# Kernel optimization log

Measured on AMD Instinct MI355X. Metric: run time of the kernel, lower is better.

## Reference

```python
import jax, jax.numpy as jnp
import numpy as np

DIM, DH, H_HEADS, F, HH, WW = 512, 64, 8, 16, 32, 32
FF_IN = int(DIM * 4 * 2 / 3)  # 1365


def _ln(x, w, b):
    m = x.mean(-1, keepdims=True)
    v = ((x - m) ** 2).mean(-1, keepdims=True)
    return (x - m) * jax.lax.rsqrt(v + 1e-5) * w + b


def _attn(x, ln_w, ln_b, wq, wkv, nkv, nbias, wout, oln_w, oln_b, rel_bias):
    # x: (B, N, D); K/V are single-head (shared across heads) per the source to_kv
    B, N, D = x.shape
    H = nbias.shape[0]
    dh = nkv.shape[-1]
    xn = _ln(x, ln_w, ln_b)
    q = (xn @ wq).reshape(B, N, H, dh).transpose(0, 2, 1, 3) * (dh ** -0.5)
    k, v = jnp.split(xn @ wkv, 2, axis=-1)  # (B, N, dh) each
    nk = jnp.broadcast_to(nkv[0], (B, 1, dh))
    nv = jnp.broadcast_to(nkv[1], (B, 1, dh))
    k = jnp.concatenate([nk, k], axis=1)  # (B, N+1, dh)
    v = jnp.concatenate([nv, v], axis=1)
    sim = jnp.einsum('bhid,bjd->bhij', q, k)  # (B, H, N, N+1)
    bias = jnp.concatenate([jnp.broadcast_to(nbias[:, None, None], (H, N, 1)), rel_bias], axis=-1)
    attn = jax.nn.softmax(sim + bias[None], axis=-1)
    out = jnp.einsum('bhij,bjd->bhid', attn, v)
    out = out.transpose(0, 2, 1, 3).reshape(B, N, H * dh)
    return _ln(out @ wout, oln_w, oln_b)


def _cpb_mlp(coords, w0, b0, w1, b1, w2, b2):
    t = jax.nn.silu(coords @ w0 + b0)
    t = jax.nn.silu(t @ w1 + b1)
    return t @ w2 + b2  # (R, heads)


def _spatial_bias(h, w, w0, b0, w1, b1, w2, b2):
    rh = jnp.arange(-h + 1, h)
    rw = jnp.arange(-w + 1, w)
    gh, gw = jnp.meshgrid(rh, rw, indexing='ij')
    coords = jnp.stack([gh, gw], axis=-1).reshape(-1, 2).astype(jnp.float32)
    table = _cpb_mlp(coords, w0, b0, w1, b1, w2, b2)  # ((2h-1)(2w-1), H)
    ph, pw = jnp.meshgrid(jnp.arange(h), jnp.arange(w), indexing='ij')
    p = jnp.stack([ph, pw], axis=-1).reshape(-1, 2)  # (hw, 2)
    rel = p[:, None] - p[None]  # (hw, hw, 2)
    idx = (rel[..., 0] + h - 1) * (2 * w - 1) + (rel[..., 1] + w - 1)
    return table[idx].transpose(2, 0, 1)  # (H, hw, hw)


def _temporal_bias(f, w0, b0, w1, b1, w2, b2):
    coords = jnp.arange(-f + 1, f, dtype=jnp.float32)[:, None]
    table = _cpb_mlp(coords, w0, b0, w1, b1, w2, b2)  # (2f-1, H)
    idx = jnp.arange(f)[:, None] - jnp.arange(f)[None] + f - 1
    return table[idx].transpose(2, 0, 1)  # (H, f, f)


def _ff(x, win, g, wout):
    # 1x1x1 conv == channel matmul; GEGLU; shift_token; ChanLayerNorm; conv out
    y = jnp.einsum('bcfhw,cd->bdfhw', x, win)
    a, gate = jnp.split(y, 2, axis=1)
    y = a * jax.nn.gelu(gate, approximate=False)
    c = y.shape[1]
    c1 = (c + 1) // 2  # torch.chunk: first chunk gets ceil
    y1, y2 = y[:, :c1], y[:, c1:]
    y2 = jnp.pad(y2, ((0, 0), (0, 0), (1, 0), (0, 0), (0, 0)))[:, :, :-1]
    y = jnp.concatenate([y1, y2], axis=1)
    m = y.mean(1, keepdims=True)
    v = ((y - m) ** 2).mean(1, keepdims=True)
    y = (y - m) * jax.lax.rsqrt(jnp.maximum(v, 1e-5)) * g.reshape(1, -1, 1, 1, 1)
    return jnp.einsum('bcfhw,cd->bdfhw', y, wout)


def setup_inputs() -> dict:
    key = jax.random.key(0)
    ks = jax.random.split(key, 32)
    d2 = DIM // 2
    inner = DH * H_HEADS

    def nrm(k, shape, s=0.02):
        return jax.random.normal(k, shape, jnp.float32) * s

    inp = {'x': jax.random.normal(ks[0], (1, DIM, F, HH, WW), jnp.float32)}
    for pre, i in (('sa', 1), ('ta', 11)):
        inp[pre + '_ln_w'] = jnp.ones(DIM, jnp.float32)
        inp[pre + '_ln_b'] = jnp.zeros(DIM, jnp.float32)
        inp[pre + '_wq'] = nrm(ks[i], (DIM, inner))
        inp[pre + '_wkv'] = nrm(ks[i + 1], (DIM, 2 * DH))
        inp[pre + '_null_kv'] = nrm(ks[i + 2], (2, DH), 1.0)
        inp[pre + '_null_bias'] = nrm(ks[i + 3], (H_HEADS,), 1.0)
        inp[pre + '_wout'] = nrm(ks[i + 4], (inner, DIM))
        inp[pre + '_oln_w'] = jnp.ones(DIM, jnp.float32)
        inp[pre + '_oln_b'] = jnp.zeros(DIM, jnp.float32)
    inp['sp_w0'] = nrm(ks[20], (2, d2), 0.1); inp['sp_b0'] = jnp.zeros(d2, jnp.float32)
    inp['sp_w1'] = nrm(ks[21], (d2, d2), 0.05); inp['sp_b1'] = jnp.zeros(d2, jnp.float32)
    inp['sp_w2'] = nrm(ks[22], (d2, H_HEADS), 0.05); inp['sp_b2'] = jnp.zeros(H_HEADS, jnp.float32)
    inp['tp_w0'] = nrm(ks[23], (1, d2), 0.1); inp['tp_b0'] = jnp.zeros(d2, jnp.float32)
    inp['tp_w1'] = nrm(ks[24], (d2, d2), 0.05); inp['tp_b1'] = jnp.zeros(d2, jnp.float32)
    inp['tp_w2'] = nrm(ks[25], (d2, H_HEADS), 0.05); inp['tp_b2'] = jnp.zeros(H_HEADS, jnp.float32)
    inp['ff_win'] = nrm(ks[26], (DIM, 2 * FF_IN))
    inp['ff_g'] = jnp.ones(FF_IN, jnp.float32)
    inp['ff_wout'] = nrm(ks[27], (FF_IN, DIM))
    return inp


def _forward(x, sa_ln_w, sa_ln_b, sa_wq, sa_wkv, sa_null_kv, sa_null_bias, sa_wout, sa_oln_w, sa_oln_b,
             ta_ln_w, ta_ln_b, ta_wq, ta_wkv, ta_null_kv, ta_null_bias, ta_wout, ta_oln_w, ta_oln_b,
             sp_w0, sp_b0, sp_w1, sp_b1, sp_w2, sp_b2,
             tp_w0, tp_b0, tp_w1, tp_b1, tp_w2, tp_b2,
             ff_win, ff_g, ff_wout):
    b, c, f, h, w = x.shape
    # spatial attention over (h*w) tokens, batched over (b*f)
    xs = x.transpose(0, 2, 3, 4, 1).reshape(b * f, h * w, c)
    sb = _spatial_bias(h, w, sp_w0, sp_b0, sp_w1, sp_b1, sp_w2, sp_b2)
    xs = _attn(xs, sa_ln_w, sa_ln_b, sa_wq, sa_wkv, sa_null_kv, sa_null_bias, sa_wout, sa_oln_w, sa_oln_b, sb) + xs
    xv = xs.reshape(b, f, h, w, c).transpose(0, 4, 1, 2, 3)
    # temporal attention over f tokens, batched over (b*h*w)
    xt = xv.transpose(0, 3, 4, 2, 1).reshape(b * h * w, f, c)
    tb = _temporal_bias(f, tp_w0, tp_b0, tp_w1, tp_b1, tp_w2, tp_b2)
    xt = _attn(xt, ta_ln_w, ta_ln_b, ta_wq, ta_wkv, ta_null_kv, ta_null_bias, ta_wout, ta_oln_w, ta_oln_b, tb) + xt
    xv = xt.reshape(b, h, w, f, c).transpose(0, 4, 3, 1, 2)
    # feed-forward with token shift
    return _ff(xv, ff_win, ff_g, ff_wout) + xv


def reference(x, sa_ln_w, sa_ln_b, sa_wq, sa_wkv, sa_null_kv, sa_null_bias, sa_wout, sa_oln_w, sa_oln_b,
              ta_ln_w, ta_ln_b, ta_wq, ta_wkv, ta_null_kv, ta_null_bias, ta_wout, ta_oln_w, ta_oln_b,
              sp_w0, sp_b0, sp_w1, sp_b1, sp_w2, sp_b2,
              tp_w0, tp_b0, tp_w1, tp_b1, tp_w2, tp_b2,
              ff_win, ff_g, ff_wout):
    return _forward(x, sa_ln_w, sa_ln_b, sa_wq, sa_wkv, sa_null_kv, sa_null_bias, sa_wout, sa_oln_w, sa_oln_b,
                    ta_ln_w, ta_ln_b, ta_wq, ta_wkv, ta_null_kv, ta_null_bias, ta_wout, ta_oln_w, ta_oln_b,
                    sp_w0, sp_b0, sp_w1, sp_b1, sp_w2, sp_b2,
                    tp_w0, tp_b0, tp_w1, tp_b1, tp_w2, tp_b2,
                    ff_win, ff_g, ff_wout)
```

## Files before the change

kernel.cpp:

```cpp
#include <hip/hip_runtime.h>
#include <math.h>

#define TOK 16384
#define DIMC 512
#define FFI 1365
#define CH1 683
#define YSLD 1376
#define KVPAD 1056
#define BSTRIDE 1152
#define MASKB (-30000.f)
#define LOG2E 1.4426950408889634f

typedef unsigned int u32;
typedef unsigned short ushort_t;
typedef __attribute__((ext_vector_type(8))) short bf16x8;
typedef __attribute__((ext_vector_type(4))) float f32x4;

__device__ inline ushort_t f2b(float x) {
    u32 u = __float_as_uint(x);
    u32 r = (u + 0x7fffu + ((u >> 16) & 1u)) >> 16;
    return (ushort_t)r;
}
__device__ inline float b2f(ushort_t u) { return __uint_as_float(((u32)u) << 16); }

__device__ inline float exp2_fast(float x) {
    float r;
    asm("v_exp_f32 %0, %1" : "=v"(r) : "v"(x));
    return r;
}

__device__ inline u32 cvt_pk_bf16(float lo, float hi) {
    u32 r;
    asm("v_cvt_pk_bf16_f32 %0, %1, %2" : "=v"(r) : "v"(lo), "v"(hi));
    return r;
}

__device__ inline void gload_lds16(const void* g, void* l) {
    __builtin_amdgcn_global_load_lds(
        (const __attribute__((address_space(1))) u32*)g,
        (__attribute__((address_space(3))) u32*)l, 16, 0, 0);
}

__device__ inline float gelu_exact(float x) {
    return 0.5f * x * (1.f + erff(x * 0.70710678118654752f));
}

__device__ inline void waitcnt_vm4() {
    asm volatile("s_waitcnt vmcnt(4)" ::: "memory");
    __builtin_amdgcn_sched_barrier(0);
}
__device__ inline void waitcnt_vm0() {
    asm volatile("s_waitcnt vmcnt(0)" ::: "memory");
    __builtin_amdgcn_sched_barrier(0);
}

__global__ __launch_bounds__(256) void cpb_kernel(
    const float* __restrict__ w0, const float* __restrict__ b0,
    const float* __restrict__ w1, const float* __restrict__ b1,
    const float* __restrict__ w2, const float* __restrict__ b2,
    float* __restrict__ table, int mode, int nrows)
{
    __shared__ float t0[16][256];
    __shared__ float t1[16][256];
    int r0 = blockIdx.x * 16;
    int t = threadIdx.x;
    float w0t = w0[t], b0t = b0[t];
    float w0t2 = (mode == 0) ? w0[256 + t] : 0.f;
    #pragma unroll
    for (int rr = 0; rr < 16; ++rr) {
        int r = r0 + rr; if (r >= nrows) r = nrows - 1;
        float c0, c1;
        if (mode == 0) { c0 = (float)(r / 63 - 31); c1 = (float)(r % 63 - 31); }
        else           { c0 = (float)(r - 15);      c1 = 0.f; }
        float a = c0 * w0t + b0t;
        if (mode == 0) a += c1 * w0t2;
        t0[rr][t] = a / (1.f + __expf(-a));
    }
    __syncthreads();
    float b1t = b1[t];
    float acc[16];
    #pragma unroll
    for (int rr = 0; rr < 16; ++rr) acc[rr] = b1t;
    for (int k = 0; k < 256; ++k) {
        float w = w1[k * 256 + t];
        #pragma unroll
        for (int rr = 0; rr < 16; ++rr) acc[rr] += t0[rr][k] * w;
    }
    #pragma unroll
    for (int rr = 0; rr < 16; ++rr) {
        float s = acc[rr];
        t1[rr][t] = s / (1.f + __expf(-s));
    }
    __syncthreads();
    if (t < 128) {
        int rr = t >> 3, oo = t & 7;
        int r = r0 + rr;
        if (r < nrows) {
            float o = b2[oo];
            for (int k = 0; k < 256; ++k) o += t1[rr][k] * w2[k * 8 + oo];
            table[r * 8 + oo] = o;
        }
    }
}

__global__ __launch_bounds__(256) void bias_sp_kernel(
    const float* __restrict__ tab, const float* __restrict__ nullbias,
    ushort_t* __restrict__ out)
{
    int pi = blockIdx.x, h = blockIdx.y;
    int phi = pi >> 5, pwi = pi & 31;
    ushort_t* row = out + ((size_t)h * 1024 + pi) * BSTRIDE;
    for (int c = threadIdx.x; c < BSTRIDE; c += 256) {
        float v;
        if (c == 0) v = nullbias[h];
        else if (c <= 1024) {
            int pj = c - 1;
            int phj = pj >> 5, pwj = pj & 31;
            int idx = (phi - phj + 31) * 63 + (pwi - pwj + 31);
            v = tab[idx * 8 + h];
        } else v = MASKB;
        row[c] = f2b(v * LOG2E);
    }
}

__global__ __launch_bounds__(256) void kvinit_kernel(
    const float* __restrict__ nullkv, ushort_t* __restrict__ KP, ushort_t* __restrict__ VT)
{
    int f = blockIdx.x, t = threadIdx.x;
    for (int e = t; e < 32 * 64; e += 256) {
        int rr = e >> 6, d = e & 63;
        int row = (rr == 0) ? 0 : (1024 + rr);
        KP[((size_t)f * KVPAD + row) * 64 + d] = (rr == 0) ? f2b(nullkv[d]) : (ushort_t)0;
    }
    for (int e = t; e < 64 * 32; e += 256) {
        int d = e >> 5, cc = e & 31;
        int col = (cc == 0) ? 0 : (1024 + cc);
        VT[((size_t)f * 64 + d) * KVPAD + col] = (cc == 0) ? f2b(nullkv[64 + d]) : (ushort_t)0;
    }
}

__global__ __launch_bounds__(256) void wcvt_kernel(
    const float* __restrict__ W, int ldw, int c0,
    ushort_t* __restrict__ Bt, int Kp, int K, int Ncols,
    const float* __restrict__ gv, int Nwrite)
{
    __shared__ float tile[32][33];
    int nb = blockIdx.x * 32, kb = blockIdx.y * 32;
    int tx = threadIdx.x & 31, ty = threadIdx.x >> 5;
    #pragma unroll
    for (int it = 0; it < 4; ++it) {
        int k = kb + ty + it * 8, n = nb + tx;
        float v = (k < K && n < Ncols) ? W[(size_t)k * ldw + c0 + n] : 0.f;
        if (gv && k < K) v *= gv[k];
        tile[ty + it * 8][tx] = v;
    }
    __syncthreads();
    #pragma unroll
    for (int it = 0; it < 4; ++it) {
        int n = nb + ty + it * 8, k = kb + tx;
        if (n < Nwrite && k < Kp) Bt[(size_t)n * Kp + k] = f2b(tile[tx][ty + it * 8]);
    }
}

__global__ __launch_bounds__(256) void transpose_in_kernel(
    const float* __restrict__ x, float* __restrict__ dst)
{
    __shared__ float tile[32][33];
    int t0b = blockIdx.x * 32, c0b = blockIdx.y * 32;
    int tx = threadIdx.x & 31, ty = threadIdx.x >> 5;
    #pragma unroll
    for (int it = 0; it < 4; ++it) {
        int c = ty + it * 8;
        tile[c][tx] = x[(size_t)(c0b + c) * TOK + t0b + tx];
    }
    __syncthreads();
    #pragma unroll
    for (int it = 0; it < 4; ++it) {
        int tr = ty + it * 8;
        dst[(size_t)(t0b + tr) * DIMC + c0b + tx] = tile[tx][tr];
    }
}

__global__ __launch_bounds__(256) void ln_bf16_kernel(
    const float* __restrict__ in, ushort_t* __restrict__ out,
    const float* __restrict__ w, const float* __restrict__ b)
{
    __shared__ float r1[4], r2[4];
    size_t base = (size_t)blockIdx.x * DIMC;
    int t = threadIdx.x;
    float x0 = in[base + t], x1 = in[base + 256 + t];
    float s = x0 + x1, s2 = x0 * x0 + x1 * x1;
    #pragma unroll
    for (int o = 32; o > 0; o >>= 1) { s += __shfl_down(s, o, 64); s2 += __shfl_down(s2, o, 64); }
    if ((t & 63) == 0) { r1[t >> 6] = s; r2[t >> 6] = s2; }
    __syncthreads();
    float mean = (r1[0] + r1[1] + r1[2] + r1[3]) * (1.f / 512.f);
    float ex2  = (r2[0] + r2[1] + r2[2] + r2[3]) * (1.f / 512.f);
    float rstd = rsqrtf(ex2 - mean * mean + 1e-5f);
    out[base + t]       = f2b((x0 - mean) * rstd * w[t] + b[t]);
    out[base + 256 + t] = f2b((x1 - mean) * rstd * w[256 + t] + b[256 + t]);
}

__global__ __launch_bounds__(256) void ln_add_sp_kernel(
    const float* __restrict__ proj, const float* __restrict__ resid,
    float* __restrict__ dstT, ushort_t* __restrict__ dstB,
    const float* __restrict__ w, const float* __restrict__ b,
    const float* __restrict__ lnw, const float* __restrict__ lnb)
{
    __shared__ float r1[4], r2[4];
    int s = blockIdx.x;
    size_t base = (size_t)s * DIMC;
    int t = threadIdx.x;
    float x0 = proj[base + t], x1 = proj[base + 256 + t];
    float sa = x0 + x1, s2 = x0 * x0 + x1 * x1;
    #pragma unroll
    for (int o = 32; o > 0; o >>= 1) { sa += __shfl_down(sa, o, 64); s2 += __shfl_down(s2, o, 64); }
    if ((t & 63) == 0) { r1[t >> 6] = sa; r2[t >> 6] = s2; }
    __syncthreads();
    float mean = (r1[0] + r1[1] + r1[2] + r1[3]) * (1.f / 512.f);
    float ex2  = (r2[0] + r2[1] + r2[2] + r2[3]) * (1.f / 512.f);
    float rstd = rsqrtf(ex2 - mean * mean + 1e-5f);
    int rd = (s & 1023) * 16 + (s >> 10);
    size_t ob = (size_t)rd * DIMC;
    float v0 = resid[base + t]       + (x0 - mean) * rstd * w[t] + b[t];
    float v1 = resid[base + 256 + t] + (x1 - mean) * rstd * w[256 + t] + b[256 + t];
    dstT[ob + t]       = v0;
    dstT[ob + 256 + t] = v1;
    __syncthreads();
    float sb = v0 + v1, sb2 = v0 * v0 + v1 * v1;
    #pragma unroll
    for (int o = 32; o > 0; o >>= 1) { sb += __shfl_down(sb, o, 64); sb2 += __shfl_down(sb2, o, 64); }
    if ((t & 63) == 0) { r1[t >> 6] = sb; r2[t >> 6] = sb2; }
    __syncthreads();
    float mean2 = (r1[0] + r1[1] + r1[2] + r1[3]) * (1.f / 512.f);
    float ex22  = (r2[0] + r2[1] + r2[2] + r2[3]) * (1.f / 512.f);
    float rstd2 = rsqrtf(ex22 - mean2 * mean2 + 1e-5f);
    dstB[ob + t]       = f2b((v0 - mean2) * rstd2 * lnw[t] + lnb[t]);
    dstB[ob + 256 + t] = f2b((v1 - mean2) * rstd2 * lnw[256 + t] + lnb[256 + t]);
}

__global__ __launch_bounds__(256) void ln_add_tp_kernel(
    const float* __restrict__ proj, const float* __restrict__ resid,
    float* __restrict__ dstF, ushort_t* __restrict__ dstB,
    const float* __restrict__ w, const float* __restrict__ b)
{
    __shared__ float r1[4], r2[4];
    int tt = blockIdx.x;
    size_t base = (size_t)tt * DIMC;
    int t = threadIdx.x;
    float x0 = proj[base + t], x1 = proj[base + 256 + t];
    float sa = x0 + x1, s2 = x0 * x0 + x1 * x1;
    #pragma unroll
    for (int o = 32; o > 0; o >>= 1) { sa += __shfl_down(sa, o, 64); s2 += __shfl_down(s2, o, 64); }
    if ((t & 63) == 0) { r1[t >> 6] = sa; r2[t >> 6] = s2; }
    __syncthreads();
    float mean = (r1[0] + r1[1] + r1[2] + r1[3]) * (1.f / 512.f);
    float ex2  = (r2[0] + r2[1] + r2[2] + r2[3]) * (1.f / 512.f);
    float rstd = rsqrtf(ex2 - mean * mean + 1e-5f);
    float v0 = resid[base + t]       + (x0 - mean) * rstd * w[t] + b[t];
    float v1 = resid[base + 256 + t] + (x1 - mean) * rstd * w[256 + t] + b[256 + t];
    int sd = (tt & 15) * 1024 + (tt >> 4);
    size_t ob = (size_t)sd * DIMC;
    dstF[ob + t]       = v0;
    dstF[ob + 256 + t] = v1;
    dstB[ob + t]       = f2b(v0);
    dstB[ob + 256 + t] = f2b(v1);
}

template<int EPI>
__global__ __launch_bounds__(256) void gemm_mfma(
    const ushort_t* __restrict__ A, int lda,
    const ushort_t* __restrict__ Bt, int Kp,
    float* __restrict__ C, ushort_t* __restrict__ Cb, int ldc,
    int M, int N, int K, float scale, int nx,
    const float* __restrict__ stats, const float* __restrict__ g,
    const float* __restrict__ resid, float* __restrict__ outT,
    ushort_t* __restrict__ KPo, ushort_t* __restrict__ VTo)
{
    __shared__ __align__(16) ushort_t As[2][4 * 128 * 8];
    __shared__ __align__(16) ushort_t Bs[2][4 * 128 * 8];
    int lin = blockIdx.x;
    int xcd = lin & 7, idx = lin >> 3;
    int m0 = (xcd * 16 + (idx & 15)) * 128;
    int n0 = (idx >> 4) * 128;
    int tid = threadIdx.x, lane = tid & 63, wid = tid >> 6;
    int wy = wid >> 1, wx = wid & 1, quad = lane >> 4, l16 = lane & 15;
    bool bfull = (n0 + 128 <= N);
    f32x4 acc[4][4];
    #pragma unroll
    for (int i = 0; i < 4; ++i)
        #pragma unroll
        for (int j = 0; j < 4; ++j) { acc[i][j][0]=0.f; acc[i][j][1]=0.f; acc[i][j][2]=0.f; acc[i][j][3]=0.f; }

    if (bfull) {
        int NT = K >> 5;
        int c0 = wid * 128 + lane, c1 = wid * 128 + 64 + lane;
        const ushort_t* gA0 = A + (size_t)(m0 + (c0 & 127)) * lda + (c0 >> 7) * 8;
        const ushort_t* gA1 = A + (size_t)(m0 + (c1 & 127)) * lda + (c1 >> 7) * 8;
        const ushort_t* gB0 = Bt + (size_t)(n0 + (c0 & 127)) * Kp + (c0 >> 7) * 8;
        const ushort_t* gB1 = Bt + (size_t)(n0 + (c1 & 127)) * Kp + (c1 >> 7) * 8;
        const int lo0 = (wid * 128) * 8, lo1 = (wid * 128 + 64) * 8;
        auto stage = [&](int buf) {
            gload_lds16(gA0, &As[buf][lo0]);
            gload_lds16(gA1, &As[buf][lo1]);
            gload_lds16(gB0, &Bs[buf][lo0]);
            gload_lds16(gB1, &Bs[buf][lo1]);
            gA0 += 32; gA1 += 32; gB0 += 32; gB1 += 32;
        };
        stage(0);
        if (NT > 1) stage(1);
        for (int t = 0; t < NT; ++t) {
            if (t + 1 < NT) waitcnt_vm4(); else waitcnt_vm0();
            __builtin_amdgcn_s_barrier();
            int cur = t & 1;
            bf16x8 af[4], bfr[4];
            #pragma unroll
            for (int i = 0; i < 4; ++i) af[i] = *(bf16x8*)&As[cur][(quad * 128 + wy * 64 + i * 16 + l16) * 8];
            #pragma unroll
            for (int j = 0; j < 4; ++j) bfr[j] = *(bf16x8*)&Bs[cur][(quad * 128 + wx * 64 + j * 16 + l16) * 8];
            #pragma unroll
            for (int i = 0; i < 4; ++i)
                #pragma unroll
                for (int j = 0; j < 4; ++j)
                    acc[i][j] = __builtin_amdgcn_mfma_f32_16x16x32_bf16(af[i], bfr[j], acc[i][j], 0, 0, 0);
            if (t + 2 < NT) {
                __builtin_amdgcn_s_barrier();
                stage(cur);
            }
        }
    } else {
        for (int k0 = 0; k0 < K; k0 += 32) {
            if (k0) __syncthreads();
            #pragma unroll
            for (int r = 0; r < 2; ++r) {
                int c = wid * 128 + r * 64 + lane;
                const ushort_t* src = A + (size_t)(m0 + (c & 127)) * lda + k0 + (c >> 7) * 8;
                gload_lds16(src, &As[0][(wid * 128 + r * 64) * 8]);
            }
            #pragma unroll
            for (int r = 0; r < 2; ++r) {
                int c = tid + r * 256;
                int kg = c >> 7, nloc = c & 127;
                bf16x8 v;
                if (n0 + nloc < N) v = *(const bf16x8*)(Bt + (size_t)(n0 + nloc) * Kp + k0 + kg * 8);
                else { for (int e = 0; e < 8; ++e) v[e] = 0; }
                *(bf16x8*)&Bs[0][c * 8] = v;
            }
            __syncthreads();
            bf16x8 af[4], bfr[4];
            #pragma unroll
            for (int i = 0; i < 4; ++i) af[i] = *(bf16x8*)&As[0][(quad * 128 + wy * 64 + i * 16 + l16) * 8];
            #pragma unroll
            for (int j = 0; j < 4; ++j) bfr[j] = *(bf16x8*)&Bs[0][(quad * 128 + wx * 64 + j * 16 + l16) * 8];
            #pragma unroll
            for (int i = 0; i < 4; ++i)
                #pragma unroll
                for (int j = 0; j < 4; ++j)
                    acc[i][j] = __builtin_amdgcn_mfma_f32_16x16x32_bf16(af[i], bfr[j], acc[i][j], 0, 0, 0);
        }
    }
    #pragma unroll
    for (int i = 0; i < 4; ++i) {
        #pragma unroll
        for (int j = 0; j < 4; ++j) {
            #pragma unroll
            for (int r = 0; r < 4; ++r) {
                int m = m0 + wy * 64 + i * 16 + quad * 4 + r;
                int n = n0 + wx * 64 + j * 16 + l16;
                if (n >= N) continue;
                float raw = acc[i][j][r];
                float v = raw * scale;
                if (EPI == 0) {
                    C[(size_t)m * ldc + n] = v;
                } else if (EPI == 3) {
                    Cb[(size_t)m * ldc + n] = f2b(v);
                } else if (EPI == 5) {
                    float s0 = stats[2 * m], s1 = stats[2 * m + 1];
                    outT[(size_t)n * TOK + m] = v * s1 - s0 * g[n] + resid[(size_t)m * DIMC + n];
                } else if (EPI == 6) {
                    if (n < 512) {
                        Cb[(size_t)m * 512 + n] = f2b(v);
                    } else {
                        int frame = m >> 10, tt = m & 1023;
                        int d = n - 512;
                        if (d < 64) KPo[((size_t)frame * KVPAD + 1 + tt) * 64 + d] = f2b(raw);
                        else        VTo[((size_t)frame * 64 + (d - 64)) * KVPAD + 1 + tt] = f2b(raw);
                    }
                } else if (EPI == 7) {
                    if (n < 512) Cb[(size_t)m * 512 + n] = f2b(v);
                    else         KPo[(size_t)m * 128 + (n - 512)] = f2b(raw);
                }
            }
        }
    }
}

__global__ __launch_bounds__(256) void ff_gemm_fused(
    const ushort_t* __restrict__ A,
    const ushort_t* __restrict__ BI,
    ushort_t* __restrict__ YS)
{
    __shared__ __align__(16) ushort_t As[2][4 * 128 * 8];
    __shared__ __align__(16) ushort_t Bs[2][4 * 2 * 64 * 8];
    int lin = blockIdx.x;
    int xcd = lin & 7, idx = lin >> 3;
    int m0 = (xcd * 16 + (idx & 15)) * 128;
    int n0 = (idx >> 4) * 64;
    int tid = threadIdx.x, lane = tid & 63, wid = tid >> 6;
    int wy = wid >> 1, wx = wid & 1, quad = lane >> 4, l16 = lane & 15;
    f32x4 aA[4][2], aG[4][2];
    #pragma unroll
    for (int i = 0; i < 4; ++i)
        #pragma unroll
        for (int j = 0; j < 2; ++j) {
            aA[i][j][0]=0.f; aA[i][j][1]=0.f; aA[i][j][2]=0.f; aA[i][j][3]=0.f;
            aG[i][j][0]=0.f; aG[i][j][1]=0.f; aG[i][j][2]=0.f; aG[i][j][3]=0.f;
        }

    int c0 = wid * 128 + lane, c1 = wid * 128 + 64 + lane;
    const ushort_t* gA0 = A + (size_t)(m0 + (c0 & 127)) * 512 + (c0 >> 7) * 8;
    const ushort_t* gA1 = A + (size_t)(m0 + (c1 & 127)) * 512 + (c1 >> 7) * 8;
    const ushort_t* gB0 = BI + (size_t)((n0 + lane) * 2 + 0) * 512 + wid * 8;
    const ushort_t* gB1 = BI + (size_t)((n0 + lane) * 2 + 1) * 512 + wid * 8;
    const int lo0 = (wid * 128) * 8, lo1 = (wid * 128 + 64) * 8;
    auto stage = [&](int buf) {
        gload_lds16(gA0, &As[buf][lo0]);
        gload_lds16(gA1, &As[buf][lo1]);
        gload_lds16(gB0, &Bs[buf][lo0]);
        gload_lds16(gB1, &Bs[buf][lo1]);
        gA0 += 32; gA1 += 32; gB0 += 32; gB1 += 32;
    };

    stage(0); stage(1);
    for (int t = 0; t < 16; ++t) {
        if (t + 1 < 16) waitcnt_vm4(); else waitcnt_vm0();
        __builtin_amdgcn_s_barrier();
        int cur = t & 1;
        bf16x8 af[4], ba[2], bg[2];
        #pragma unroll
        for (int i = 0; i < 4; ++i) af[i] = *(bf16x8*)&As[cur][(quad * 128 + wy * 64 + i * 16 + l16) * 8];
        #pragma unroll
        for (int j = 0; j < 2; ++j) {
            int nn = wx * 32 + j * 16 + l16;
            ba[j] = *(bf16x8*)&Bs[cur][(quad * 128 + nn) * 8];
            bg[j] = *(bf16x8*)&Bs[cur][(quad * 128 + 64 + nn) * 8];
        }
        #pragma unroll
        for (int i = 0; i < 4; ++i)
            #pragma unroll
            for (int j = 0; j < 2; ++j) {
                aA[i][j] = __builtin_amdgcn_mfma_f32_16x16x32_bf16(af[i], ba[j], aA[i][j], 0, 0, 0);
                aG[i][j] = __builtin_amdgcn_mfma_f32_16x16x32_bf16(af[i], bg[j], aG[i][j], 0, 0, 0);
            }
        if (t + 2 < 16) {
            __builtin_amdgcn_s_barrier();
            stage(cur);
        }
    }
    #pragma unroll
    for (int i = 0; i < 4; ++i) {
        #pragma unroll
        for (int j = 0; j < 2; ++j) {
            #pragma unroll
            for (int r = 0; r < 4; ++r) {
                int m = m0 + wy * 64 + i * 16 + quad * 4 + r;
                int n = n0 + wx * 32 + j * 16 + l16;
                if (n >= FFI) {
                    if (n < YSLD) YS[(size_t)m * YSLD + n] = 0;
                    continue;
                }
                float v = aA[i][j][r] * gelu_exact(aG[i][j][r]);
                int dr = (n < CH1) ? m : m + 1024;
                if (dr < TOK) YS[(size_t)dr * YSLD + n] = f2b(v);
                if (n >= CH1 && m < 1024) YS[(size_t)m * YSLD + n] = 0;
            }
        }
    }
}

__global__ __launch_bounds__(256) void attn_sp_mfma(
    const ushort_t* __restrict__ Q,
    const ushort_t* __restrict__ KP,
    const ushort_t* __restrict__ VT,
    const ushort_t* __restrict__ BIASX,
    ushort_t* __restrict__ O)
{
    __shared__ __align__(16) ushort_t Ks[128 * 64];
    __shared__ __align__(16) ushort_t Vs[64 * 128];
    int lin = blockIdx.x;
    int xcd = lin & 7, idx = lin >> 3;
    int qt = xcd * 8 + (idx & 7);
    int frame = idx >> 3;
    int q0 = qt * 16;
    int tid = threadIdx.x, lane = tid & 63, wid = tid >> 6;
    int quad = lane >> 4, l16 = lane & 15;

    bf16x8 aQ[2][2];
    const ushort_t* brow[2];
    #pragma unroll
    for (int i = 0; i < 2; ++i) {
        int h = wid * 2 + i;
        const ushort_t* qp = Q + (size_t)(frame * 1024 + q0 + l16) * 512 + h * 64 + quad * 8;
        aQ[i][0] = *(const bf16x8*)qp;
        aQ[i][1] = *(const bf16x8*)(qp + 32);
        brow[i] = BIASX + ((size_t)h * 1024 + q0 + l16) * BSTRIDE;
    }
    f32x4 Oc[2][4];
    f32x4 Oc4[2];
    #pragma unroll
    for (int i = 0; i < 2; ++i) {
        #pragma unroll
        for (int nt = 0; nt < 4; ++nt) { Oc[i][nt][0]=0.f; Oc[i][nt][1]=0.f; Oc[i][nt][2]=0.f; Oc[i][nt][3]=0.f; }
        Oc4[i][0]=0.f; Oc4[i][1]=0.f; Oc4[i][2]=0.f; Oc4[i][3]=0.f;
    }
    bf16x8 vones;
    #pragma unroll
    for (int e = 0; e < 8; ++e) vones[e] = (short)0x3F80;

    int idxA = (((quad & 1) * 32) + l16) * 4;
    int idxB = idxA + 64;
    bool hiq = (quad >= 2);

    for (int jt = 0; jt < 9; ++jt) {
        __syncthreads();
        #pragma unroll
        for (int r = 0; r < 4; ++r) {
            int L = wid * 256 + r * 64 + lane;
            int c = L >> 3, gp = L & 7, gg = gp ^ (c & 7);
            int jj = jt * 128 + c; if (jj > KVPAD - 1) jj = KVPAD - 1;
            gload_lds16(KP + ((size_t)frame * KVPAD + jj) * 64 + gg * 8, &Ks[(wid * 256 + r * 64) * 8]);
        }
        #pragma unroll
        for (int r = 0; r < 4; ++r) {
            int L = wid * 256 + r * 64 + lane;
            int d = L >> 4, cgp = L & 15;
            int cg = (cgp & 8) | ((cgp & 7) ^ (d & 7));
            int col = jt * 128 + cg * 8; if (col > KVPAD - 8) col = KVPAD - 8;
            gload_lds16(VT + ((size_t)frame * 64 + d) * KVPAD + col, &Vs[(wid * 256 + r * 64) * 8]);
        }
        __syncthreads();

        #pragma unroll
        for (int i = 0; i < 2; ++i) {
            f32x4 S[8];
            #pragma unroll
            for (int j = 0; j < 8; ++j) { S[j][0]=0.f; S[j][1]=0.f; S[j][2]=0.f; S[j][3]=0.f; }
            __builtin_amdgcn_s_setprio(1);
            #pragma unroll
            for (int j = 0; j < 8; ++j) {
                int c = j * 16 + l16;
                #pragma unroll
                for (int ks = 0; ks < 2; ++ks) {
                    bf16x8 kb = *(bf16x8*)&Ks[(c * 8 + ((ks * 4 + quad) ^ (c & 7))) * 8];
                    S[j] = __builtin_amdgcn_mfma_f32_16x16x32_bf16(kb, aQ[i][ks], S[j], 0, 0, 0);
                }
            }
            __builtin_amdgcn_s_setprio(0);
            #pragma unroll
            for (int j = 0; j < 8; ++j) {
                int kbase = jt * 128 + j * 16 + quad * 4;
                uint2 bv = *(const uint2*)(brow[i] + kbase);
                S[j][0] = exp2_fast(S[j][0] + __uint_as_float(bv.x << 16));
                S[j][1] = exp2_fast(S[j][1] + __uint_as_float(bv.x & 0xffff0000u));
                S[j][2] = exp2_fast(S[j][2] + __uint_as_float(bv.y << 16));
                S[j][3] = exp2_fast(S[j][3] + __uint_as_float(bv.y & 0xffff0000u));
            }
            __builtin_amdgcn_s_setprio(1);
            #pragma unroll
            for (int ks = 0; ks < 4; ++ks) {
                int jl = 2 * ks, jh = 2 * ks + 1;
                u32 pxl = cvt_pk_bf16(S[jl][0], S[jl][1]);
                u32 pyl = cvt_pk_bf16(S[jl][2], S[jl][3]);
                u32 pxh = cvt_pk_bf16(S[jh][0], S[jh][1]);
                u32 pyh = cvt_pk_bf16(S[jh][2], S[jh][3]);
                u32 a0 = (u32)__builtin_amdgcn_ds_bpermute(idxA, (int)pxl);
                u32 a1 = (u32)__builtin_amdgcn_ds_bpermute(idxA, (int)pxh);
                u32 b0 = (u32)__builtin_amdgcn_ds_bpermute(idxA, (int)pyl);
                u32 b1 = (u32)__builtin_amdgcn_ds_bpermute(idxA, (int)pyh);
                u32 c0 = (u32)__builtin_amdgcn_ds_bpermute(idxB, (int)pxl);
                u32 c1 = (u32)__builtin_amdgcn_ds_bpermute(idxB, (int)pxh);
                u32 d0 = (u32)__builtin_amdgcn_ds_bpermute(idxB, (int)pyl);
                u32 d1 = (u32)__builtin_amdgcn_ds_bpermute(idxB, (int)pyh);
                union { u32 w[4]; bf16x8 v; } pa;
                pa.w[0] = hiq ? a1 : a0;
                pa.w[1] = hiq ? b1 : b0;
                pa.w[2] = hiq ? c1 : c0;
                pa.w[3] = hiq ? d1 : d0;
                #pragma unroll
                for (int nt = 0; nt < 4; ++nt) {
                    int d = nt * 16 + l16;
                    int cg = ks * 4 + quad;
                    int phys = (cg & 8) | ((cg & 7) ^ (d & 7));
                    bf16x8 vb = *(bf16x8*)&Vs[(d * 16 + phys) * 8];
                    Oc[i][nt] = __builtin_amdgcn_mfma_f32_16x16x32_bf16(pa.v, vb, Oc[i][nt], 0, 0, 0);
                }
                Oc4[i] = __builtin_amdgcn_mfma_f32_16x16x32_bf16(pa.v, vones, Oc4[i], 0, 0, 0);
            }
            __builtin_amdgcn_s_setprio(0);
        }
    }
    #pragma unroll
    for (int i = 0; i < 2; ++i) {
        int h = wid * 2 + i;
        #pragma unroll
        for (int r = 0; r < 4; ++r) {
            float linv = 1.f / Oc4[i][r];
            int ql = quad * 4 + r;
            #pragma unroll
            for (int nt = 0; nt < 4; ++nt) {
                int d = nt * 16 + l16;
                O[(size_t)(frame * 1024 + q0 + ql) * 512 + h * 64 + d] = f2b(Oc[i][nt][r] * linv);
            }
        }
    }
}

__global__ __launch_bounds__(256) void attn_tp_kernel(
    const ushort_t* __restrict__ q, const ushort_t* __restrict__ kv,
    const float* __restrict__ nullkv, const float* __restrict__ nullbias,
    const float* __restrict__ table, ushort_t* __restrict__ out)
{
    __shared__ float qs[16][516];
    __shared__ float ks[17][68];
    __shared__ float vs[17][68];
    __shared__ float sc[8][16][17];
    int b = blockIdx.x;
    int t = threadIdx.x;
    for (int e = t; e < 16 * 64; e += 256) {
        int f = e >> 6, c8 = e & 63;
        uint4 v = *(const uint4*)(q + (size_t)(b * 16 + f) * 512 + c8 * 8);
        float* dst = &qs[f][c8 * 8];
        dst[0] = b2f((ushort_t)(v.x & 0xffffu)); dst[1] = b2f((ushort_t)(v.x >> 16));
        dst[2] = b2f((ushort_t)(v.y & 0xffffu)); dst[3] = b2f((ushort_t)(v.y >> 16));
        dst[4] = b2f((ushort_t)(v.z & 0xffffu)); dst[5] = b2f((ushort_t)(v.z >> 16));
        dst[6] = b2f((ushort_t)(v.w & 0xffffu)); dst[7] = b2f((ushort_t)(v.w >> 16));
    }
    for (int e = t; e < 17 * 64; e += 256) {
        int j = e >> 6, d = e & 63;
        ks[j][d] = (j == 0) ? nullkv[d]      : b2f(kv[(size_t)(b * 16 + j - 1) * 128 + d]);
        vs[j][d] = (j == 0) ? nullkv[64 + d] : b2f(kv[(size_t)(b * 16 + j - 1) * 128 + 64 + d]);
    }
    __syncthreads();
    for (int e = t; e < 8 * 16 * 17; e += 256) {
        int h = e / 272, rem = e - h * 272;
        int i = rem / 17, j = rem - i * 17;
        float acc = 0.f;
        const float4* qp = (const float4*)&qs[i][h * 64];
        const float4* kp = (const float4*)&ks[j][0];
        #pragma unroll
        for (int d4 = 0; d4 < 16; ++d4) {
            float4 qv = qp[d4], kv4 = kp[d4];
            acc += qv.x * kv4.x;
            acc += qv.y * kv4.y;
            acc += qv.z * kv4.z;
            acc += qv.w * kv4.w;
        }
        float bias = ((j == 0) ? nullbias[h] : table[(i - (j - 1) + 15) * 8 + h]) * LOG2E;
        sc[h][i][j] = acc + bias;
    }
    __syncthreads();
    if (t < 128) {
        int h = t >> 4, i = t & 15;
        float mx = -1e30f;
        for (int j = 0; j < 17; ++j) mx = fmaxf(mx, sc[h][i][j]);
        float s = 0.f;
        for (int j = 0; j < 17; ++j) { float p = exp2_fast(sc[h][i][j] - mx); sc[h][i][j] = p; s += p; }
        float inv = 1.f / s;
        for (int j = 0; j < 17; ++j) sc[h][i][j] *= inv;
    }
    __syncthreads();
    for (int e = t; e < 16 * 128; e += 256) {
        int i = e >> 7, c4 = e & 127;
        int h = c4 >> 4, d4 = c4 & 15;
        float ax = 0.f, ay = 0.f, az = 0.f, aw = 0.f;
        #pragma unroll
        for (int j = 0; j < 17; ++j) {
            float p = sc[h][i][j];
            float4 vv = *(const float4*)&vs[j][d4 * 4];
            ax += p * vv.x; ay += p * vv.y; az += p * vv.z; aw += p * vv.w;
        }
        u32 lo = (u32)f2b(ax) | ((u32)f2b(ay) << 16);
        u32 hi = (u32)f2b(az) | ((u32)f2b(aw) << 16);
        *(uint2*)(out + (size_t)(b * 16 + i) * 512 + c4 * 4) = make_uint2(lo, hi);
    }
}

__global__ __launch_bounds__(256) void rowstats_bf16_kernel(
    const ushort_t* __restrict__ YS, float* __restrict__ stats)
{
    __shared__ float r1[4], r2[4];
    int r = blockIdx.x, t = threadIdx.x;
    const ushort_t* row = YS + (size_t)r * YSLD;
    float s = 0.f, s2 = 0.f;
    for (int c = t; c < FFI; c += 256) {
        float v = b2f(row[c]);
        s += v; s2 += v * v;
    }
    #pragma unroll
    for (int o = 32; o > 0; o >>= 1) { s += __shfl_down(s, o, 64); s2 += __shfl_down(s2, o, 64); }
    if ((t & 63) == 0) { r1[t >> 6] = s; r2[t >> 6] = s2; }
    __syncthreads();
    float S  = r1[0] + r1[1] + r1[2] + r1[3];
    float S2 = r2[0] + r2[1] + r2[2] + r2[3];
    float mean = S * (1.f / 1365.f);
    float var  = S2 * (1.f / 1365.f) - mean * mean;
    float rstd = rsqrtf(fmaxf(var, 1e-5f));
    if (t == 0) { stats[2 * r] = mean * rstd; stats[2 * r + 1] = rstd; }
}

__global__ __launch_bounds__(64) void colsum_kernel(
    const ushort_t* __restrict__ Wt, float* __restrict__ colsum)
{
    int n = blockIdx.x, t = threadIdx.x;
    const ushort_t* row = Wt + (size_t)n * YSLD;
    float s = 0.f;
    for (int k = t; k < YSLD; k += 64) s += b2f(row[k]);
    #pragma unroll
    for (int o = 32; o > 0; o >>= 1) s += __shfl_down(s, o, 64);
    if (t == 0) colsum[n] = s;
}

extern "C" void kernel_launch(void* const* d_in, const int* in_sizes, int n_in,
                              void* d_out, int out_size, void* d_ws, size_t ws_size,
                              hipStream_t stream)
{
    const float* x          = (const float*)d_in[0];
    const float* sa_ln_w    = (const float*)d_in[1];
    const float* sa_ln_b    = (const float*)d_in[2];
    const float* sa_wq      = (const float*)d_in[3];
    const float* sa_wkv     = (const float*)d_in[4];
    const float* sa_null_kv = (const float*)d_in[5];
    const float* sa_null_b  = (const float*)d_in[6];
    const float* sa_wout    = (const float*)d_in[7];
    const float* sa_oln_w   = (const float*)d_in[8];
    const float* sa_oln_b   = (const float*)d_in[9];
    const float* ta_ln_w    = (const float*)d_in[10];
    const float* ta_ln_b    = (const float*)d_in[11];
    const float* ta_wq      = (const float*)d_in[12];
    const float* ta_wkv     = (const float*)d_in[13];
    const float* ta_null_kv = (const float*)d_in[14];
    const float* ta_null_b  = (const float*)d_in[15];
    const float* ta_wout    = (const float*)d_in[16];
    const float* ta_oln_w   = (const float*)d_in[17];
    const float* ta_oln_b   = (const float*)d_in[18];
    const float* sp_w0      = (const float*)d_in[19];
    const float* sp_b0      = (const float*)d_in[20];
    const float* sp_w1      = (const float*)d_in[21];
    const float* sp_b1      = (const float*)d_in[22];
    const float* sp_w2      = (const float*)d_in[23];
    const float* sp_b2      = (const float*)d_in[24];
    const float* tp_w0      = (const float*)d_in[25];
    const float* tp_b0      = (const float*)d_in[26];
    const float* tp_w1      = (const float*)d_in[27];
    const float* tp_b1      = (const float*)d_in[28];
    const float* tp_w2      = (const float*)d_in[29];
    const float* tp_b2      = (const float*)d_in[30];
    const float* ff_win     = (const float*)d_in[31];
    const float* ff_g       = (const float*)d_in[32];
    const float* ff_wout    = (const float*)d_in[33];

    char* ws = (char*)d_ws;
    float*    RES   = (float*)(ws + 0);
    ushort_t* XN16  = (ushort_t*)(ws + 33554432);
    ushort_t* Q16   = (ushort_t*)(ws + 50331648);
    float*    RT    = (float*)(ws + 50331648);
    ushort_t* YS    = (ushort_t*)(ws + 50331648);
    ushort_t* WSA   = (ushort_t*)(ws + 67108864);
    ushort_t* KP    = (ushort_t*)(ws + 83886080);
    ushort_t* VTb   = (ushort_t*)(ws + 86048768);
    ushort_t* KV16  = (ushort_t*)(ws + 83886080);
    ushort_t* WTA   = (ushort_t*)(ws + 90439680);
    ushort_t* AO16  = (ushort_t*)(ws + 92274688);
    ushort_t* BI    = (ushort_t*)(ws + 96468992);
    ushort_t* WFFB  = (ushort_t*)(ws + 99352576);
    ushort_t* BIAS16= (ushort_t*)(ws + 109051904);
    float*    PRJ   = (float*)(ws + 109051904);
    ushort_t* Q16t  = (ushort_t*)(ws + 109051904);
    float*    STATS = (float*)(ws + 142606336);
    float*    SPT   = (float*)(ws + 142737408);
    float*    COLSUM= (float*)(ws + 142737408);
    float*    TPT   = (float*)(ws + 142864448);

    ushort_t* WQ_T  = WSA;
    ushort_t* WKV_T = WSA + 262144;
    ushort_t* WO_T  = WSA + 327680;
    ushort_t* tWQ_T  = WTA;
    ushort_t* tWKV_T = WTA + 262144;
    ushort_t* tWO_T  = WTA + 327680;

    dim3 blk(256);
    const float QSCL = 0.125f * LOG2E;

    cpb_kernel<<<dim3(249), blk, 0, stream>>>(sp_w0, sp_b0, sp_w1, sp_b1, sp_w2, sp_b2, SPT, 0, 3969);
    cpb_kernel<<<dim3(2),   blk, 0, stream>>>(tp_w0, tp_b0, tp_w1, tp_b1, tp_w2, tp_b2, TPT, 1, 31);
    bias_sp_kernel<<<dim3(1024, 8), blk, 0, stream>>>(SPT, sa_null_b, BIAS16);
    kvinit_kernel<<<dim3(16), blk, 0, stream>>>(sa_null_kv, KP, VTb);

    wcvt_kernel<<<dim3(16, 16), blk, 0, stream>>>(sa_wq, 512, 0, WQ_T, 512, 512, 512, nullptr, 512);
    wcvt_kernel<<<dim3(4, 16),  blk, 0, stream>>>(sa_wkv, 128, 0, WKV_T, 512, 512, 128, nullptr, 128);
    wcvt_kernel<<<dim3(16, 16), blk, 0, stream>>>(sa_wout, 512, 0, WO_T, 512, 512, 512, nullptr, 512);
    transpose_in_kernel<<<dim3(512, 16), blk, 0, stream>>>(x, RES);
    ln_bf16_kernel<<<dim3(TOK), blk, 0, stream>>>(RES, XN16, sa_ln_w, sa_ln_b);
    gemm_mfma<6><<<dim3(640), blk, 0, stream>>>(XN16, 512, WQ_T, 512,
        nullptr, Q16, 512, TOK, 640, 512, QSCL, 5, nullptr, nullptr, nullptr, nullptr, KP, VTb);
    attn_sp_mfma<<<dim3(1024), blk, 0, stream>>>(Q16, KP, VTb, BIAS16, AO16);
    gemm_mfma<0><<<dim3(512), blk, 0, stream>>>(AO16, 512, WO_T, 512,
        PRJ, nullptr, 512, TOK, 512, 512, 1.0f, 4, nullptr, nullptr, nullptr, nullptr, nullptr, nullptr);
    ln_add_sp_kernel<<<dim3(TOK), blk, 0, stream>>>(PRJ, RES, RT, XN16, sa_oln_w, sa_oln_b, ta_ln_w, ta_ln_b);

    wcvt_kernel<<<dim3(16, 16), blk, 0, stream>>>(ta_wq, 512, 0, tWQ_T, 512, 512, 512, nullptr, 512);
    wcvt_kernel<<<dim3(4, 16),  blk, 0, stream>>>(ta_wkv, 128, 0, tWKV_T, 512, 512, 128, nullptr, 128);
    wcvt_kernel<<<dim3(16, 16), blk, 0, stream>>>(ta_wout, 512, 0, tWO_T, 512, 512, 512, nullptr, 512);
    gemm_mfma<7><<<dim3(640), blk, 0, stream>>>(XN16, 512, tWQ_T, 512,
        nullptr, Q16t, 512, TOK, 640, 512, QSCL, 5, nullptr, nullptr, nullptr, nullptr, KV16, nullptr);
    attn_tp_kernel<<<dim3(1024), blk, 0, stream>>>(Q16t, KV16, ta_null_kv, ta_null_b, TPT, AO16);
    gemm_mfma<0><<<dim3(512), blk, 0, stream>>>(AO16, 512, tWO_T, 512,
        PRJ, nullptr, 512, TOK, 512, 512, 1.0f, 4, nullptr, nullptr, nullptr, nullptr, nullptr, nullptr);
    ln_add_tp_kernel<<<dim3(TOK), blk, 0, stream>>>(PRJ, RT, RES, XN16, ta_oln_w, ta_oln_b);

    wcvt_kernel<<<dim3(44, 16), blk, 0, stream>>>(ff_win, 2730, 0,   BI,       1024, 512, FFI, nullptr, 1408);
    wcvt_kernel<<<dim3(44, 16), blk, 0, stream>>>(ff_win, 2730, FFI, BI + 512, 1024, 512, FFI, nullptr, 1408);
    wcvt_kernel<<<dim3(16, 43), blk, 0, stream>>>(ff_wout, 512, 0, WFFB, YSLD, FFI, 512, ff_g, 512);
    colsum_kernel<<<dim3(512), dim3(64), 0, stream>>>(WFFB, COLSUM);
    ff_gemm_fused<<<dim3(2816), blk, 0, stream>>>(XN16, BI, YS);
    rowstats_bf16_kernel<<<dim3(TOK), blk, 0, stream>>>(YS, STATS);
    gemm_mfma<5><<<dim3(512), blk, 0, stream>>>(YS, YSLD, WFFB, YSLD,
        nullptr, nullptr, 0, TOK, 512, YSLD, 1.0f, 4, STATS, COLSUM, RES, (float*)d_out, nullptr, nullptr);
}
```

Measured before the change: 765.4 us.

## Load GEMM B fragments directly into registers, bypassing LDS staging

In the generic GEMM and the fused feed-forward GEMM, the B operand is no longer staged through shared memory. Each wave now loads its own B fragments from global memory straight into registers, one k-step ahead, using two register sets that alternate. The A tile still goes through double-buffered LDS, and the wait counts are adjusted to match the new number of loads in flight. This cuts LDS traffic and shared-memory footprint, but waves with the same column range now fetch the same B data separately, and the per-lane 16-byte global reads are less coalesced.

Measured after the change: 935.2 us. 22.2% more time.

```diff
diff --git a/kernel.cpp b/kernel.cpp
--- a/kernel.cpp
+++ b/kernel.cpp
@@ -47,6 +47,10 @@
 
 __device__ inline void waitcnt_vm4() {
     asm volatile("s_waitcnt vmcnt(4)" ::: "memory");
+    __builtin_amdgcn_sched_barrier(0);
+}
+__device__ inline void waitcnt_vm2() {
+    asm volatile("s_waitcnt vmcnt(2)" ::: "memory");
     __builtin_amdgcn_sched_barrier(0);
 }
 __device__ inline void waitcnt_vm0() {
@@ -297,37 +301,41 @@
         int c0 = wid * 128 + lane, c1 = wid * 128 + 64 + lane;
         const ushort_t* gA0 = A + (size_t)(m0 + (c0 & 127)) * lda + (c0 >> 7) * 8;
         const ushort_t* gA1 = A + (size_t)(m0 + (c1 & 127)) * lda + (c1 >> 7) * 8;
-        const ushort_t* gB0 = Bt + (size_t)(n0 + (c0 & 127)) * Kp + (c0 >> 7) * 8;
-        const ushort_t* gB1 = Bt + (size_t)(n0 + (c1 & 127)) * Kp + (c1 >> 7) * 8;
         const int lo0 = (wid * 128) * 8, lo1 = (wid * 128 + 64) * 8;
-        auto stage = [&](int buf) {
+        auto stageA = [&](int buf) {
             gload_lds16(gA0, &As[buf][lo0]);
             gload_lds16(gA1, &As[buf][lo1]);
-            gload_lds16(gB0, &Bs[buf][lo0]);
-            gload_lds16(gB1, &Bs[buf][lo1]);
-            gA0 += 32; gA1 += 32; gB0 += 32; gB1 += 32;
+            gA0 += 32; gA1 += 32;
         };
-        stage(0);
-        if (NT > 1) stage(1);
-        for (int t = 0; t < NT; ++t) {
-            if (t + 1 < NT) waitcnt_vm4(); else waitcnt_vm0();
+        const ushort_t* gBbase = Bt + (size_t)(n0 + wx * 64 + l16) * Kp + quad * 8;
+        bf16x8 rb0[4], rb1[4];
+        auto loadB = [&](bf16x8 (&br)[4], int k0) {
+            #pragma unroll
+            for (int j = 0; j < 4; ++j)
+                br[j] = *(const bf16x8*)(gBbase + (size_t)j * 16 * Kp + k0);
+        };
+        auto iterbody = [&](int t, bf16x8 (&bc)[4], bf16x8 (&bn)[4]) {
+            if (t == 0 || t == NT - 1) waitcnt_vm0(); else waitcnt_vm2();
             __builtin_amdgcn_s_barrier();
+            if (t + 1 < NT) loadB(bn, (t + 1) * 32);
             int cur = t & 1;
-            bf16x8 af[4], bfr[4];
+            bf16x8 af[4];
             #pragma unroll
             for (int i = 0; i < 4; ++i) af[i] = *(bf16x8*)&As[cur][(quad * 128 + wy * 64 + i * 16 + l16) * 8];
-            #pragma unroll
-            for (int j = 0; j < 4; ++j) bfr[j] = *(bf16x8*)&Bs[cur][(quad * 128 + wx * 64 + j * 16 + l16) * 8];
             #pragma unroll
             for (int i = 0; i < 4; ++i)
                 #pragma unroll
                 for (int j = 0; j < 4; ++j)
-                    acc[i][j] = __builtin_amdgcn_mfma_f32_16x16x32_bf16(af[i], bfr[j], acc[i][j], 0, 0, 0);
-            if (t + 2 < NT) {
-                __builtin_amdgcn_s_barrier();
-                stage(cur);
-            }
-        }
+                    acc[i][j] = __builtin_amdgcn_mfma_f32_16x16x32_bf16(af[i], bc[j], acc[i][j], 0, 0, 0);
+            __builtin_amdgcn_s_barrier();
+            if (t + 2 < NT) stageA(cur);
+        };
+        stageA(0);
+        if (NT > 1) stageA(1);
+        loadB(rb0, 0);
+        int t = 0;
+        for (; t + 1 < NT; t += 2) { iterbody(t, rb0, rb1); iterbody(t + 1, rb1, rb0); }
+        if (t < NT) iterbody(t, rb0, rb1);
     } else {
         for (int k0 = 0; k0 < K; k0 += 32) {
             if (k0) __syncthreads();
@@ -401,7 +409,6 @@
     ushort_t* __restrict__ YS)
 {
     __shared__ __align__(16) ushort_t As[2][4 * 128 * 8];
-    __shared__ __align__(16) ushort_t Bs[2][4 * 2 * 64 * 8];
     int lin = blockIdx.x;
     int xcd = lin & 7, idx = lin >> 3;
     int m0 = (xcd * 16 + (idx & 15)) * 128;
@@ -420,42 +427,48 @@
     int c0 = wid * 128 + lane, c1 = wid * 128 + 64 + lane;
     const ushort_t* gA0 = A + (size_t)(m0 + (c0 & 127)) * 512 + (c0 >> 7) * 8;
     const ushort_t* gA1 = A + (size_t)(m0 + (c1 & 127)) * 512 + (c1 >> 7) * 8;
-    const ushort_t* gB0 = BI + (size_t)((n0 + lane) * 2 + 0) * 512 + wid * 8;
-    const ushort_t* gB1 = BI + (size_t)((n0 + lane) * 2 + 1) * 512 + wid * 8;
     const int lo0 = (wid * 128) * 8, lo1 = (wid * 128 + 64) * 8;
-    auto stage = [&](int buf) {
+    auto stageA = [&](int buf) {
         gload_lds16(gA0, &As[buf][lo0]);
         gload_lds16(gA1, &As[buf][lo1]);
-        gload_lds16(gB0, &Bs[buf][lo0]);
-        gload_lds16(gB1, &Bs[buf][lo1]);
-        gA0 += 32; gA1 += 32; gB0 += 32; gB1 += 32;
+        gA0 += 32; gA1 += 32;
     };
-
-    stage(0); stage(1);
-    for (int t = 0; t < 16; ++t) {
-        if (t + 1 < 16) waitcnt_vm4(); else waitcnt_vm0();
+    int nnb = n0 + wx * 32 + l16;
+    const ushort_t* gBa = BI + (size_t)(nnb * 2 + 0) * 512 + quad * 8;
+    const ushort_t* gBg = BI + (size_t)(nnb * 2 + 1) * 512 + quad * 8;
+    bf16x8 a0f[2], g0f[2], a1f[2], g1f[2];
+    auto loadB = [&](bf16x8 (&ba)[2], bf16x8 (&bg)[2], int k0) {
+        #pragma unroll
+        for (int j = 0; j < 2; ++j) {
+            ba[j] = *(const bf16x8*)(gBa + (size_t)j * 16384 + k0);
+            bg[j] = *(const bf16x8*)(gBg + (size_t)j * 16384 + k0);
+        }
+    };
+    auto iterbody = [&](int t, bf16x8 (&bca)[2], bf16x8 (&bcg)[2],
+                        bf16x8 (&bna)[2], bf16x8 (&bng)[2]) {
+        if (t == 0 || t == 15) waitcnt_vm0(); else waitcnt_vm2();
         __builtin_amdgcn_s_barrier();
+        if (t + 1 < 16) loadB(bna, bng, (t + 1) * 32);
         int cur = t & 1;
-        bf16x8 af[4], ba[2], bg[2];
+        bf16x8 af[4];
         #pragma unroll
         for (int i = 0; i < 4; ++i) af[i] = *(bf16x8*)&As[cur][(quad * 128 + wy * 64 + i * 16 + l16) * 8];
         #pragma unroll
-        for (int j = 0; j < 2; ++j) {
-            int nn = wx * 32 + j * 16 + l16;
-            ba[j] = *(bf16x8*)&Bs[cur][(quad * 128 + nn) * 8];
-            bg[j] = *(bf16x8*)&Bs[cur][(quad * 128 + 64 + nn) * 8];
-        }
-        #pragma unroll
         for (int i = 0; i < 4; ++i)
             #pragma unroll
             for (int j = 0; j < 2; ++j) {
-                aA[i][j] = __builtin_amdgcn_mfma_f32_16x16x32_bf16(af[i], ba[j], aA[i][j], 0, 0, 0);
-                aG[i][j] = __builtin_amdgcn_mfma_f32_16x16x32_bf16(af[i], bg[j], aG[i][j], 0, 0, 0);
+                aA[i][j] = __builtin_amdgcn_mfma_f32_16x16x32_bf16(af[i], bca[j], aA[i][j], 0, 0, 0);
+                aG[i][j] = __builtin_amdgcn_mfma_f32_16x16x32_bf16(af[i], bcg[j], aG[i][j], 0, 0, 0);
             }
-        if (t + 2 < 16) {
-            __builtin_amdgcn_s_barrier();
-            stage(cur);
-        }
+        __builtin_amdgcn_s_barrier();
+        if (t + 2 < 16) stageA(cur);
+    };
+    stageA(0); stageA(1);
+    loadB(a0f, g0f, 0);
+    #pragma unroll
+    for (int t = 0; t < 16; t += 2) {
+        iterbody(t, a0f, g0f, a1f, g1f);
+        iterbody(t + 1, a1f, g1f, a0f, g0f);
     }
     #pragma unroll
     for (int i = 0; i < 4; ++i) {
```
